# Optimization experiments

Hardware: AMD Instinct MI355X
Metric: run time of the kernel (lower is better)

The kernel has to match this reference:

```python
import jax, jax.numpy as jnp
import numpy as np

N_NODES = 100000
N_EDGES = 3200000
IN_FEAT = 512
HIDDEN = 256
N_CLASS = 40


def setup_inputs() -> dict:
    key = jax.random.key(0)
    ks = jax.random.split(key, 6)
    x = jax.random.normal(ks[0], (N_NODES, IN_FEAT), dtype=jnp.float32)
    w1 = jax.random.uniform(ks[1], (IN_FEAT, HIDDEN), dtype=jnp.float32)
    b1 = jnp.zeros((HIDDEN,), dtype=jnp.float32)
    w2 = jax.random.uniform(ks[2], (HIDDEN, N_CLASS), dtype=jnp.float32)
    b2 = jnp.zeros((N_CLASS,), dtype=jnp.float32)
    edge_val = jax.random.uniform(ks[3], (N_EDGES,), dtype=jnp.float32)
    edge_row = jax.random.randint(ks[4], (N_EDGES,), 0, N_NODES, dtype=jnp.int32)
    edge_col = jax.random.randint(ks[5], (N_EDGES,), 0, N_NODES, dtype=jnp.int32)
    return {"x": x, "w1": w1, "b1": b1, "w2": w2, "b2": b2,
            "edge_val": edge_val, "edge_row": edge_row, "edge_col": edge_col}


def _graph_conv(h, w, b, edge_val, edge_row, edge_col, n_nodes):
    # dense transform: [N, d_in] @ [d_in, d_out]
    support = h @ w
    # sparse adj @ support via gather + segment_sum (COO SpMM)
    msgs = edge_val[:, None] * support[edge_col]          # [E, d_out]
    agg = jax.ops.segment_sum(msgs, edge_row, num_segments=n_nodes)
    return agg + b


def reference(x, w1, b1, w2, b2, edge_val, edge_row, edge_col):
    n = x.shape[0]
    h = jax.nn.relu(_graph_conv(x, w1, b1, edge_val, edge_row, edge_col, n))
    # dropout is identity in eval mode (training=False)
    out = _graph_conv(h, w2, b2, edge_val, edge_row, edge_col, n)
    return jax.nn.log_softmax(out, axis=1)
```

## Files before the change

kernel.cpp:

```cpp
#include <hip/hip_runtime.h>
#include <cstdint>
#include <cstddef>

#define N_NODES 100000
#define N_EDGES 3200000
#define IN_FEAT 512
#define HIDDEN  256
#define N_CLASS 40
#define S2_STRIDE 48

#define N_BUCKETS 196
#define SC_CHUNK 4096
#define N_SC_BLOCKS 782

#define OFF_SUPPORT1 ((size_t)0)
#define OFF_H        ((size_t)51200000)
#define OFF_SUPPORT2 ((size_t)102400000)
#define OFF_W1T      ((size_t)112000000)
#define OFF_RPTR     ((size_t)112262144)
#define OFF_BCNT     ((size_t)112662272)
#define OFF_BBASE    ((size_t)112663296)
#define OFF_BCUR     ((size_t)112664320)
#define OFF_BINNED   ((size_t)112665344)
#define OFF_SEDGE    ((size_t)138265344)

typedef __attribute__((ext_vector_type(8))) short short8x;
typedef __attribute__((ext_vector_type(4))) float f32x4;
typedef __attribute__((ext_vector_type(8))) unsigned short u16x8;
typedef __attribute__((ext_vector_type(3))) unsigned int u32x3;
typedef __attribute__((ext_vector_type(4))) unsigned int u32x4;

static __device__ __forceinline__ unsigned short f2bf(float f) {
  unsigned u = __float_as_uint(f);
  unsigned r = (u + 0x7FFFu + ((u >> 16) & 1u)) >> 16;
  return (unsigned short)r;
}
static __device__ __forceinline__ float bf2f(unsigned short s) {
  return __uint_as_float(((unsigned)s) << 16);
}
static __device__ __forceinline__ float bflo(unsigned u) {
  return __uint_as_float(u << 16);
}
static __device__ __forceinline__ float bfhi(unsigned u) {
  return __uint_as_float(u & 0xFFFF0000u);
}

__global__ __launch_bounds__(256) void k_bincnt(const int* __restrict__ erow,
                                                int* __restrict__ bcnt,
                                                const float* __restrict__ W,
                                                unsigned short* __restrict__ Wt) {
  int tid = blockIdx.x * 256 + threadIdx.x;
  {
    int n = tid & 255;
    int k = tid >> 8;
    Wt[(size_t)n * IN_FEAT + k] = f2bf(W[(size_t)k * HIDDEN + n]);
  }
  __shared__ int lh[256];
  lh[threadIdx.x] = 0;
  __syncthreads();
  int i = tid;
  int stride = gridDim.x * blockDim.x;
  for (; i < N_EDGES; i += stride) atomicAdd(&lh[erow[i] >> 9], 1);
  __syncthreads();
  if (threadIdx.x < N_BUCKETS) atomicAdd(&bcnt[threadIdx.x], lh[threadIdx.x]);
}

__global__ __launch_bounds__(256) void k_binscan(const int* __restrict__ bcnt,
                                                 int* __restrict__ bbase,
                                                 int* __restrict__ bcur,
                                                 int* __restrict__ rptr) {
  __shared__ int s[256];
  int t = threadIdx.x;
  int v = (t < N_BUCKETS) ? bcnt[t] : 0;
  s[t] = v;
  __syncthreads();
  for (int off = 1; off < 256; off <<= 1) {
    int y = (t >= off) ? s[t - off] : 0;
    __syncthreads();
    s[t] += y;
    __syncthreads();
  }
  if (t < N_BUCKETS) {
    int e = s[t] - v;
    bbase[t] = e;
    bcur[t] = e;
  }
  if (t == 0) {
    bbase[N_BUCKETS] = N_EDGES;
    rptr[N_NODES] = N_EDGES;
  }
}

__global__ __launch_bounds__(256) void k_binscatter(const int* __restrict__ erow,
                                                    const int* __restrict__ ecol,
                                                    const float* __restrict__ eval,
                                                    int* __restrict__ bcur,
                                                    int2* __restrict__ binned) {
  __shared__ int lcnt[256];
  __shared__ int lcur[256];
  const int t = threadIdx.x;
  const int base = blockIdx.x * SC_CHUNK;
  lcnt[t] = 0;
  __syncthreads();
  int rows[16], cols[16], vals[16];
#pragma unroll
  for (int e = 0; e < 16; e++) {
    int i = base + t + e * 256;
    if (i < N_EDGES) {
      rows[e] = erow[i];
      cols[e] = ecol[i];
      vals[e] = __float_as_int(eval[i]);
      atomicAdd(&lcnt[rows[e] >> 9], 1);
    } else {
      rows[e] = -1;
    }
  }
  __syncthreads();
  if (t < N_BUCKETS) lcur[t] = atomicAdd(&bcur[t], lcnt[t]);
  __syncthreads();
#pragma unroll
  for (int e = 0; e < 16; e++) {
    if (rows[e] >= 0) {
      int bkt = rows[e] >> 9;
      int p = atomicAdd(&lcur[bkt], 1);
      binned[p] = make_int2(((rows[e] & 511) << 17) | cols[e], vals[e]);
    }
  }
}

__global__ __launch_bounds__(256) void k_bucket_csr(const int2* __restrict__ binned,
                                                    const int* __restrict__ bbase,
                                                    int* __restrict__ rptr,
                                                    int2* __restrict__ sedge) {
  const int b = blockIdx.x;
  const int t = threadIdx.x;
  __shared__ int cnt[512];
  __shared__ int excl[512];
  __shared__ int s[256];
  cnt[t] = 0;
  cnt[t + 256] = 0;
  __syncthreads();
  const int ebase = bbase[b];
  const int ecnt = bbase[b + 1] - ebase;
  for (int i = t; i < ecnt; i += 256)
    atomicAdd(&cnt[((unsigned)binned[ebase + i].x) >> 17], 1);
  __syncthreads();
  int c0 = cnt[2 * t], c1 = cnt[2 * t + 1];
  s[t] = c0 + c1;
  __syncthreads();
  for (int off = 1; off < 256; off <<= 1) {
    int y = (t >= off) ? s[t - off] : 0;
    __syncthreads();
    s[t] += y;
    __syncthreads();
  }
  int e = s[t] - (c0 + c1);
  excl[2 * t] = e;
  excl[2 * t + 1] = e + c0;
  __syncthreads();
  for (int i = t; i < 512; i += 256) {
    int node = b * 512 + i;
    if (node < N_NODES) rptr[node] = ebase + excl[i];
  }
  __syncthreads();
  for (int i = t; i < ecnt; i += 256) {
    int2 e2 = binned[ebase + i];
    int lrow = ((unsigned)e2.x) >> 17;
    int col = e2.x & 0x1FFFF;
    int p = atomicAdd(&excl[lrow], 1);
    sedge[ebase + p] = make_int2(col, e2.y);
  }
}

__global__ __launch_bounds__(256) void k_gemm1(const float* __restrict__ X,
                                               const unsigned short* __restrict__ Wt,
                                               unsigned short* __restrict__ C) {
  __shared__ short As[128 * 32];
  __shared__ short Bs[256 * 32];
  const int t = threadIdx.x;
  const int wave = t >> 6, lane = t & 63;
  const int q = lane >> 4, r = lane & 15;
  const int wm = (wave >> 1) * 64;
  const int wn = (wave & 1) * 128;
  const int m0 = blockIdx.x * 128;

  f32x4 acc[4][8];
#pragma unroll
  for (int mi = 0; mi < 4; mi++)
#pragma unroll
    for (int ni = 0; ni < 8; ni++) acc[mi][ni] = (f32x4){0.f, 0.f, 0.f, 0.f};

  for (int k0 = 0; k0 < IN_FEAT; k0 += 32) {
#pragma unroll
    for (int i = 0; i < 2; i++) {
      int cidx = t + i * 256;
      int row = cidx >> 2;
      int ko = (cidx & 3) * 8;
      int gr = m0 + row;
      if (gr > N_NODES - 1) gr = N_NODES - 1;
      const float4* src = (const float4*)&X[(size_t)gr * IN_FEAT + k0 + ko];
      float4 x0 = src[0], x1 = src[1];
      short8x a;
      a[0] = (short)f2bf(x0.x); a[1] = (short)f2bf(x0.y);
      a[2] = (short)f2bf(x0.z); a[3] = (short)f2bf(x0.w);
      a[4] = (short)f2bf(x1.x); a[5] = (short)f2bf(x1.y);
      a[6] = (short)f2bf(x1.z); a[7] = (short)f2bf(x1.w);
      *(short8x*)&As[row * 32 + ko] = a;
    }
#pragma unroll
    for (int i = 0; i < 4; i++) {
      int cidx = t + i * 256;
      int row = cidx >> 2;
      int ko = (cidx & 3) * 8;
      short8x b = *(const short8x*)&Wt[(size_t)row * IN_FEAT + k0 + ko];
      *(short8x*)&Bs[row * 32 + ko] = b;
    }
    __syncthreads();
    short8x af[4], bf[8];
#pragma unroll
    for (int mi = 0; mi < 4; mi++)
      af[mi] = *(const short8x*)&As[(wm + mi * 16 + r) * 32 + q * 8];
#pragma unroll
    for (int ni = 0; ni < 8; ni++)
      bf[ni] = *(const short8x*)&Bs[(wn + ni * 16 + r) * 32 + q * 8];
#pragma unroll
    for (int mi = 0; mi < 4; mi++)
#pragma unroll
      for (int ni = 0; ni < 8; ni++)
        acc[mi][ni] = __builtin_amdgcn_mfma_f32_16x16x32_bf16(af[mi], bf[ni],
                                                              acc[mi][ni], 0, 0, 0);
    __syncthreads();
  }
#pragma unroll
  for (int mi = 0; mi < 4; mi++) {
#pragma unroll
    for (int ni = 0; ni < 8; ni++) {
      int col = wn + ni * 16 + r;
#pragma unroll
      for (int reg = 0; reg < 4; reg++) {
        int row = m0 + wm + mi * 16 + q * 4 + reg;
        if (row < N_NODES)
          C[(size_t)row * HIDDEN + col] = f2bf(acc[mi][ni][reg]);
      }
    }
  }
}

__global__ __launch_bounds__(256) void k_spmm1(const unsigned short* __restrict__ S,
                                               const int* __restrict__ rptr,
                                               const int2* __restrict__ sedge,
                                               const float* __restrict__ b1,
                                               unsigned short* __restrict__ H) {
  const int node = (blockIdx.x * blockDim.x + threadIdx.x) >> 6;
  const int lane = threadIdx.x & 63;
  const int half = lane >> 5;
  const int fl = lane & 31;
  int e0 = rptr[node], e1 = rptr[node + 1];
  float a[8];
#pragma unroll
  for (int k = 0; k < 8; k++) a[k] = 0.f;
  for (int base = e0; base < e1; base += 64) {
    int rem = min(64, e1 - base);
    int c = 0;
    float v = 0.f;
    if (lane < rem) {
      int2 e = sedge[base + lane];
      c = e.x;
      v = __int_as_float(e.y);
    }
    int iters = (rem + 1) >> 1;
#pragma unroll 8
    for (int j = 0; j < iters; j++) {
      int idx = 2 * j + half;
      int cj = __shfl(c, idx);
      float vj = __shfl(v, idx);
      short8x s8 = *(const short8x*)&S[(size_t)cj * HIDDEN + fl * 8];
#pragma unroll
      for (int k = 0; k < 8; k++)
        a[k] += vj * bf2f((unsigned short)s8[k]);
    }
  }
#pragma unroll
  for (int k = 0; k < 8; k++) a[k] += __shfl_xor(a[k], 32);
  if (half == 0) {
    float4 b0 = *(const float4*)&b1[fl * 8];
    float4 b4 = *(const float4*)&b1[fl * 8 + 4];
    u16x8 o;
    o[0] = f2bf(fmaxf(a[0] + b0.x, 0.f));
    o[1] = f2bf(fmaxf(a[1] + b0.y, 0.f));
    o[2] = f2bf(fmaxf(a[2] + b0.z, 0.f));
    o[3] = f2bf(fmaxf(a[3] + b0.w, 0.f));
    o[4] = f2bf(fmaxf(a[4] + b4.x, 0.f));
    o[5] = f2bf(fmaxf(a[5] + b4.y, 0.f));
    o[6] = f2bf(fmaxf(a[6] + b4.z, 0.f));
    o[7] = f2bf(fmaxf(a[7] + b4.w, 0.f));
    *(u16x8*)&H[(size_t)node * HIDDEN + fl * 8] = o;
  }
}

__global__ __launch_bounds__(256) void k_gemm2(const unsigned short* __restrict__ H,
                                               const float* __restrict__ W2,
                                               unsigned short* __restrict__ S2) {
  __shared__ __align__(16) float Ws[HIDDEN][N_CLASS];
  __shared__ float Hs[256][33];
  const int t = threadIdx.x;
  const int r0 = blockIdx.x * 256;

#pragma unroll
  for (int i = 0; i < 10; i++) {
    int qq = t + i * 256;
    float4 w = *(const float4*)&W2[(size_t)qq * 4];
    *(float4*)&((float*)Ws)[(size_t)qq * 4] = w;
  }

  float acc[N_CLASS];
#pragma unroll
  for (int n = 0; n < N_CLASS; n++) acc[n] = 0.f;

  for (int kc = 0; kc < HIDDEN; kc += 32) {
    __syncthreads();
#pragma unroll
    for (int i = 0; i < 8; i++) {
      int qq = t + i * 256;
      int row = qq >> 3;
      int kv = (qq & 7) * 4;
      int grow = r0 + row;
      if (grow > N_NODES - 1) grow = N_NODES - 1;
      ushort4 hv = *(const ushort4*)&H[(size_t)grow * HIDDEN + kc + kv];
      Hs[row][kv + 0] = bf2f(hv.x);
      Hs[row][kv + 1] = bf2f(hv.y);
      Hs[row][kv + 2] = bf2f(hv.z);
      Hs[row][kv + 3] = bf2f(hv.w);
    }
    __syncthreads();
    const float4* Wsv = (const float4*)Ws;
#pragma unroll
    for (int k = 0; k < 32; k++) {
      float hk = Hs[t][k];
      int kg = kc + k;
#pragma unroll
      for (int n4 = 0; n4 < 10; n4++) {
        float4 w = Wsv[kg * 10 + n4];
        acc[n4 * 4 + 0] += hk * w.x;
        acc[n4 * 4 + 1] += hk * w.y;
        acc[n4 * 4 + 2] += hk * w.z;
        acc[n4 * 4 + 3] += hk * w.w;
      }
    }
  }
  int row = r0 + t;
  if (row < N_NODES) {
    unsigned pk[24];
#pragma unroll
    for (int i = 0; i < 20; i++)
      pk[i] = (unsigned)f2bf(acc[2 * i]) | ((unsigned)f2bf(acc[2 * i + 1]) << 16);
#pragma unroll
    for (int i = 20; i < 24; i++) pk[i] = 0;
    unsigned* dst = (unsigned*)&S2[(size_t)row * S2_STRIDE];
#pragma unroll
    for (int i = 0; i < 6; i++) {
      u32x4 o = {pk[4 * i], pk[4 * i + 1], pk[4 * i + 2], pk[4 * i + 3]};
      *(u32x4*)&dst[4 * i] = o;
    }
  }
}

__global__ __launch_bounds__(256) void k_spmm2(const unsigned short* __restrict__ S2,
                                               const int* __restrict__ rptr,
                                               const int2* __restrict__ sedge,
                                               const float* __restrict__ b2,
                                               float* __restrict__ out) {
  const int node = (blockIdx.x * blockDim.x + threadIdx.x) >> 6;
  const int lane = threadIdx.x & 63;
  const int q = lane >> 3;
  const int fl = lane & 7;
  int e0 = rptr[node], e1 = rptr[node + 1];
  float a[6] = {0.f, 0.f, 0.f, 0.f, 0.f, 0.f};
  for (int base = e0; base < e1; base += 64) {
    int rem = min(64, e1 - base);
    int c = 0;
    float v = 0.f;
    if (lane < rem) {
      int2 e = sedge[base + lane];
      c = e.x;
      v = __int_as_float(e.y);
    }
    int iters = (rem + 7) >> 3;
#pragma unroll 4
    for (int j = 0; j < iters; j++) {
      int idx = 8 * j + q;
      int cj = __shfl(c, idx);
      float vj = __shfl(v, idx);
      u32x3 w = *(const u32x3*)&S2[(size_t)cj * S2_STRIDE + fl * 6];
      a[0] += vj * bflo(w.x);
      a[1] += vj * bfhi(w.x);
      a[2] += vj * bflo(w.y);
      a[3] += vj * bfhi(w.y);
      a[4] += vj * bflo(w.z);
      a[5] += vj * bfhi(w.z);
    }
  }
#pragma unroll
  for (int k = 0; k < 6; k++) {
    a[k] += __shfl_xor(a[k], 8);
    a[k] += __shfl_xor(a[k], 16);
    a[k] += __shfl_xor(a[k], 32);
  }
  float x[6];
  float mloc = -INFINITY;
#pragma unroll
  for (int k = 0; k < 6; k++) {
    int f = fl * 6 + k;
    x[k] = (f < N_CLASS) ? (a[k] + b2[f]) : -INFINITY;
    mloc = fmaxf(mloc, x[k]);
  }
#pragma unroll
  for (int o = 1; o < 8; o <<= 1) mloc = fmaxf(mloc, __shfl_xor(mloc, o));
  float sloc = 0.f;
#pragma unroll
  for (int k = 0; k < 6; k++)
    sloc += (fl * 6 + k < N_CLASS) ? expf(x[k] - mloc) : 0.f;
#pragma unroll
  for (int o = 1; o < 8; o <<= 1) sloc += __shfl_xor(sloc, o);
  float ls = logf(sloc);
  if (q == 0) {
#pragma unroll
    for (int k = 0; k < 6; k++) {
      int f = fl * 6 + k;
      if (f < N_CLASS) out[(size_t)node * N_CLASS + f] = (x[k] - mloc) - ls;
    }
  }
}

extern "C" void kernel_launch(void* const* d_in, const int* in_sizes, int n_in,
                              void* d_out, int out_size, void* d_ws, size_t ws_size,
                              hipStream_t stream) {
  const float* x    = (const float*)d_in[0];
  const float* w1   = (const float*)d_in[1];
  const float* b1   = (const float*)d_in[2];
  const float* w2   = (const float*)d_in[3];
  const float* b2   = (const float*)d_in[4];
  const float* eval = (const float*)d_in[5];
  const int*   erow = (const int*)d_in[6];
  const int*   ecol = (const int*)d_in[7];
  float* out = (float*)d_out;

  char* ws = (char*)d_ws;
  unsigned short* support1 = (unsigned short*)(ws + OFF_SUPPORT1);
  unsigned short* h        = (unsigned short*)(ws + OFF_H);
  unsigned short* support2 = (unsigned short*)(ws + OFF_SUPPORT2);
  unsigned short* w1t = (unsigned short*)(ws + OFF_W1T);
  int*   rptr   = (int*)(ws + OFF_RPTR);
  int*   bcnt   = (int*)(ws + OFF_BCNT);
  int*   bbase  = (int*)(ws + OFF_BBASE);
  int*   bcur   = (int*)(ws + OFF_BCUR);
  int2*  binned = (int2*)(ws + OFF_BINNED);
  int2*  sedge  = (int2*)(ws + OFF_SEDGE);

  hipMemsetAsync(bcnt, 0, N_BUCKETS * 4, stream);
  k_bincnt<<<512, 256, 0, stream>>>(erow, bcnt, w1, w1t);
  k_binscan<<<1, 256, 0, stream>>>(bcnt, bbase, bcur, rptr);
  k_binscatter<<<N_SC_BLOCKS, 256, 0, stream>>>(erow, ecol, eval, bcur, binned);
  k_bucket_csr<<<N_BUCKETS, 256, 0, stream>>>(binned, bbase, rptr, sedge);

  k_gemm1<<<dim3((N_NODES + 127) / 128, 1), 256, 0, stream>>>(x, w1t, support1);
  k_spmm1<<<N_NODES / 4, 256, 0, stream>>>(support1, rptr, sedge, b1, h);

  k_gemm2<<<(N_NODES + 255) / 256, 256, 0, stream>>>(h, w2, support2);
  k_spmm2<<<N_NODES / 4, 256, 0, stream>>>(support2, rptr, sedge, b2, out);
}
```

Before: 860.8 us.

## Rewrite second dense GEMM with bf16 MFMA and pre-transposed W2

The scalar-FMA second GEMM, which staged data through LDS, is replaced by a per-wave bf16 MFMA 16x16x32 kernel. It reads H directly and uses a transposed, zero-padded bf16 copy of W2 that k_bincnt now builds. The first SpMM is split into two launches over node halves, and the unroll factor in spmm2 is raised. The GEMM2 change cuts scalar FMA and LDS work but rounds W2 to bf16, and it writes S2 with scattered 2-byte stores.

```diff
diff --git a/kernel.cpp b/kernel.cpp
--- a/kernel.cpp
+++ b/kernel.cpp
@@ -17,12 +17,13 @@
 #define OFF_H        ((size_t)51200000)
 #define OFF_SUPPORT2 ((size_t)102400000)
 #define OFF_W1T      ((size_t)112000000)
-#define OFF_RPTR     ((size_t)112262144)
-#define OFF_BCNT     ((size_t)112662272)
-#define OFF_BBASE    ((size_t)112663296)
-#define OFF_BCUR     ((size_t)112664320)
-#define OFF_BINNED   ((size_t)112665344)
-#define OFF_SEDGE    ((size_t)138265344)
+#define OFF_W2T      ((size_t)112262144)
+#define OFF_RPTR     ((size_t)112286976)
+#define OFF_BCNT     ((size_t)112687104)
+#define OFF_BBASE    ((size_t)112688128)
+#define OFF_BCUR     ((size_t)112689152)
+#define OFF_BINNED   ((size_t)112690176)
+#define OFF_SEDGE    ((size_t)138290176)
 
 typedef __attribute__((ext_vector_type(8))) short short8x;
 typedef __attribute__((ext_vector_type(4))) float f32x4;
@@ -47,13 +48,20 @@
 
 __global__ __launch_bounds__(256) void k_bincnt(const int* __restrict__ erow,
                                                 int* __restrict__ bcnt,
-                                                const float* __restrict__ W,
-                                                unsigned short* __restrict__ Wt) {
+                                                const float* __restrict__ W1,
+                                                unsigned short* __restrict__ W1t,
+                                                const float* __restrict__ W2,
+                                                unsigned short* __restrict__ W2t) {
   int tid = blockIdx.x * 256 + threadIdx.x;
   {
     int n = tid & 255;
     int k = tid >> 8;
-    Wt[(size_t)n * IN_FEAT + k] = f2bf(W[(size_t)k * HIDDEN + n]);
+    W1t[(size_t)n * IN_FEAT + k] = f2bf(W1[(size_t)k * HIDDEN + n]);
+  }
+  if (tid < 48 * HIDDEN) {
+    int n = tid >> 8;
+    int k = tid & 255;
+    W2t[n * HIDDEN + k] = (n < N_CLASS) ? f2bf(W2[(size_t)k * N_CLASS + n]) : 0;
   }
   __shared__ int lh[256];
   lh[threadIdx.x] = 0;
@@ -250,8 +258,9 @@
                                                const int* __restrict__ rptr,
                                                const int2* __restrict__ sedge,
                                                const float* __restrict__ b1,
-                                               unsigned short* __restrict__ H) {
-  const int node = (blockIdx.x * blockDim.x + threadIdx.x) >> 6;
+                                               unsigned short* __restrict__ H,
+                                               int node_off) {
+  const int node = node_off + ((blockIdx.x * blockDim.x + threadIdx.x) >> 6);
   const int lane = threadIdx.x & 63;
   const int half = lane >> 5;
   const int fl = lane & 31;
@@ -299,68 +308,38 @@
 }
 
 __global__ __launch_bounds__(256) void k_gemm2(const unsigned short* __restrict__ H,
-                                               const float* __restrict__ W2,
+                                               const unsigned short* __restrict__ W2t,
                                                unsigned short* __restrict__ S2) {
-  __shared__ __align__(16) float Ws[HIDDEN][N_CLASS];
-  __shared__ float Hs[256][33];
   const int t = threadIdx.x;
-  const int r0 = blockIdx.x * 256;
-
-#pragma unroll
-  for (int i = 0; i < 10; i++) {
-    int qq = t + i * 256;
-    float4 w = *(const float4*)&W2[(size_t)qq * 4];
-    *(float4*)&((float*)Ws)[(size_t)qq * 4] = w;
-  }
-
-  float acc[N_CLASS];
-#pragma unroll
-  for (int n = 0; n < N_CLASS; n++) acc[n] = 0.f;
-
-  for (int kc = 0; kc < HIDDEN; kc += 32) {
-    __syncthreads();
-#pragma unroll
-    for (int i = 0; i < 8; i++) {
-      int qq = t + i * 256;
-      int row = qq >> 3;
-      int kv = (qq & 7) * 4;
-      int grow = r0 + row;
-      if (grow > N_NODES - 1) grow = N_NODES - 1;
-      ushort4 hv = *(const ushort4*)&H[(size_t)grow * HIDDEN + kc + kv];
-      Hs[row][kv + 0] = bf2f(hv.x);
-      Hs[row][kv + 1] = bf2f(hv.y);
-      Hs[row][kv + 2] = bf2f(hv.z);
-      Hs[row][kv + 3] = bf2f(hv.w);
-    }
-    __syncthreads();
-    const float4* Wsv = (const float4*)Ws;
-#pragma unroll
-    for (int k = 0; k < 32; k++) {
-      float hk = Hs[t][k];
-      int kg = kc + k;
-#pragma unroll
-      for (int n4 = 0; n4 < 10; n4++) {
-        float4 w = Wsv[kg * 10 + n4];
-        acc[n4 * 4 + 0] += hk * w.x;
-        acc[n4 * 4 + 1] += hk * w.y;
-        acc[n4 * 4 + 2] += hk * w.z;
-        acc[n4 * 4 + 3] += hk * w.w;
-      }
-    }
-  }
-  int row = r0 + t;
-  if (row < N_NODES) {
-    unsigned pk[24];
-#pragma unroll
-    for (int i = 0; i < 20; i++)
-      pk[i] = (unsigned)f2bf(acc[2 * i]) | ((unsigned)f2bf(acc[2 * i + 1]) << 16);
-#pragma unroll
-    for (int i = 20; i < 24; i++) pk[i] = 0;
-    unsigned* dst = (unsigned*)&S2[(size_t)row * S2_STRIDE];
-#pragma unroll
-    for (int i = 0; i < 6; i++) {
-      u32x4 o = {pk[4 * i], pk[4 * i + 1], pk[4 * i + 2], pk[4 * i + 3]};
-      *(u32x4*)&dst[4 * i] = o;
+  const int wave = t >> 6, lane = t & 63;
+  const int q = lane >> 4, r = lane & 15;
+  const int m0 = blockIdx.x * 64 + wave * 16;
+
+  f32x4 acc[3];
+#pragma unroll
+  for (int n = 0; n < 3; n++) acc[n] = (f32x4){0.f, 0.f, 0.f, 0.f};
+
+  int arow = m0 + r;
+  if (arow > N_NODES - 1) arow = N_NODES - 1;
+  const unsigned short* Arow = &H[(size_t)arow * HIDDEN + q * 8];
+
+#pragma unroll
+  for (int k0 = 0; k0 < HIDDEN; k0 += 32) {
+    short8x af = *(const short8x*)&Arow[k0];
+    short8x bf0 = *(const short8x*)&W2t[(0 * 16 + r) * HIDDEN + k0 + q * 8];
+    short8x bf1 = *(const short8x*)&W2t[(1 * 16 + r) * HIDDEN + k0 + q * 8];
+    short8x bf2 = *(const short8x*)&W2t[(2 * 16 + r) * HIDDEN + k0 + q * 8];
+    acc[0] = __builtin_amdgcn_mfma_f32_16x16x32_bf16(af, bf0, acc[0], 0, 0, 0);
+    acc[1] = __builtin_amdgcn_mfma_f32_16x16x32_bf16(af, bf1, acc[1], 0, 0, 0);
+    acc[2] = __builtin_amdgcn_mfma_f32_16x16x32_bf16(af, bf2, acc[2], 0, 0, 0);
+  }
+#pragma unroll
+  for (int n = 0; n < 3; n++) {
+#pragma unroll
+    for (int reg = 0; reg < 4; reg++) {
+      int row = m0 + q * 4 + reg;
+      if (row < N_NODES)
+        S2[(size_t)row * S2_STRIDE + n * 16 + r] = f2bf(acc[n][reg]);
     }
   }
 }
@@ -386,7 +365,7 @@
       v = __int_as_float(e.y);
     }
     int iters = (rem + 7) >> 3;
-#pragma unroll 4
+#pragma unroll 8
     for (int j = 0; j < iters; j++) {
       int idx = 8 * j + q;
       int cj = __shfl(c, idx);
@@ -450,6 +429,7 @@
   unsigned short* h        = (unsigned short*)(ws + OFF_H);
   unsigned short* support2 = (unsigned short*)(ws + OFF_SUPPORT2);
   unsigned short* w1t = (unsigned short*)(ws + OFF_W1T);
+  unsigned short* w2t = (unsigned short*)(ws + OFF_W2T);
   int*   rptr   = (int*)(ws + OFF_RPTR);
   int*   bcnt   = (int*)(ws + OFF_BCNT);
   int*   bbase  = (int*)(ws + OFF_BBASE);
@@ -458,14 +438,15 @@
   int2*  sedge  = (int2*)(ws + OFF_SEDGE);
 
   hipMemsetAsync(bcnt, 0, N_BUCKETS * 4, stream);
-  k_bincnt<<<512, 256, 0, stream>>>(erow, bcnt, w1, w1t);
+  k_bincnt<<<512, 256, 0, stream>>>(erow, bcnt, w1, w1t, w2, w2t);
   k_binscan<<<1, 256, 0, stream>>>(bcnt, bbase, bcur, rptr);
   k_binscatter<<<N_SC_BLOCKS, 256, 0, stream>>>(erow, ecol, eval, bcur, binned);
   k_bucket_csr<<<N_BUCKETS, 256, 0, stream>>>(binned, bbase, rptr, sedge);
 
   k_gemm1<<<dim3((N_NODES + 127) / 128, 1), 256, 0, stream>>>(x, w1t, support1);
-  k_spmm1<<<N_NODES / 4, 256, 0, stream>>>(support1, rptr, sedge, b1, h);
-
-  k_gemm2<<<(N_NODES + 255) / 256, 256, 0, stream>>>(h, w2, support2);
+  k_spmm1<<<N_NODES / 8, 256, 0, stream>>>(support1, rptr, sedge, b1, h, 0);
+  k_spmm1<<<N_NODES / 8, 256, 0, stream>>>(support1, rptr, sedge, b1, h, N_NODES / 2);
+
+  k_gemm2<<<(N_NODES + 63) / 64, 256, 0, stream>>>(h, w2t, support2);
   k_spmm2<<<N_NODES / 4, 256, 0, stream>>>(support2, rptr, sedge, b2, out);
 }
```

Result: faster. 803.3 us (-6.7%).
